# Performance work log

Hardware: AMD Instinct MI355X
Metric: run time of the kernel (lower is better)

The kernel has to match this reference:

```python
import jax, jax.numpy as jnp
import numpy as np

N_CAM = 6
N_HEADS = 8
N_POINTS = 4
D = 256  # internal d_model of the deformable attention


def _sine_pos(h, w, d=D):
    # DETR PositionEmbeddingSine, normalize=True, channels-last (h, w, d)
    npf = d // 2
    two_pi = 2.0 * np.pi
    y = jnp.arange(1, h + 1, dtype=jnp.float32) / (h + 1e-6) * two_pi
    x = jnp.arange(1, w + 1, dtype=jnp.float32) / (w + 1e-6) * two_pi
    dim_t = (10000.0 ** (2.0 * (jnp.arange(npf) // 2) / npf)).astype(jnp.float32)
    def enc(v):
        p = v[:, None] / dim_t
        return jnp.stack([jnp.sin(p[:, 0::2]), jnp.cos(p[:, 1::2])], axis=-1).reshape(v.shape[0], -1)
    py, px = enc(y), enc(x)
    return jnp.concatenate([
        jnp.broadcast_to(py[:, None, :], (h, w, npf)),
        jnp.broadcast_to(px[None, :, :], (h, w, npf))], axis=-1)


def _layernorm(x, g, b, eps=1e-5):
    mu = jnp.mean(x, -1, keepdims=True)
    var = jnp.mean((x - mu) ** 2, -1, keepdims=True)
    return (x - mu) * jax.lax.rsqrt(var + eps) * g + b


def _bilinear_gather(kv, loc_x, loc_y, H, W):
    # kv: (b, L, heads, H*W, c); loc_*: (b, Lq, heads, L, P) normalized to [0,1]
    # emulates F.grid_sample(mode='bilinear', padding_mode='zeros', align_corners=False)
    b, L, heads, HW, c = kv.shape
    _, Lq, _, _, P = loc_x.shape
    x = loc_x * W - 0.5
    y = loc_y * H - 0.5
    x0 = jnp.floor(x)
    y0 = jnp.floor(y)
    fx = x - x0
    fy = y - y0
    out = jnp.zeros((b, Lq, heads, L, P, c), kv.dtype)
    for dx in (0, 1):
        for dy in (0, 1):
            xi = x0 + dx
            yi = y0 + dy
            valid = (xi >= 0) & (xi < W) & (yi >= 0) & (yi < H)
            wgt = (fx if dx else 1.0 - fx) * (fy if dy else 1.0 - fy) * valid
            idx = (jnp.clip(yi, 0, H - 1) * W + jnp.clip(xi, 0, W - 1)).astype(jnp.int32)
            idx_t = idx.transpose(0, 3, 2, 1, 4).reshape(b, L, heads, Lq * P, 1)
            g = jnp.take_along_axis(kv, idx_t, axis=3)
            g = g.reshape(b, L, heads, Lq, P, c).transpose(0, 3, 2, 1, 4, 5)
            out = out + wgt[..., None] * g
    return out  # (b, Lq, heads, L, P, c)


def reference(x, conv0_w, conv0_b, conv2_w, conv2_b, cam_emb,
              off_w, off_b, val_w, val_b, key_w, key_b, out_w, out_b,
              conv1_w, conv1_b, norm0_g, norm0_b,
              lin1_w, lin1_b, lin2_w, lin2_b, norm2_g, norm2_b):
    bn, dim, H, W = x.shape
    b = bn // N_CAM
    hd = D // N_HEADS
    HW = H * W
    Lq = N_CAM * HW

    x_nhwc = x.transpose(0, 2, 3, 1)                  # (bn, H, W, dim)
    residual = x_nhwc.reshape(b, Lq, dim)             # b (n h w) d

    src = (x_nhwc @ conv0_w.T + conv0_b).reshape(b, N_CAM, H, W, D)  # conv0 1x1

    pos = _sine_pos(H, W)                              # (H, W, 256)
    spc = src + pos[None, None] + cam_emb[None, :, None, None, :]
    # per-level global descriptor: mean over pixels of conv2(src+pos+cam)
    g = jnp.mean((spc @ conv2_w.T + conv2_b).reshape(b, N_CAM, HW, D), axis=2)  # (b, n, 256)

    src_flat = src.reshape(b, Lq, D)
    query = spc.reshape(b, Lq, D)                      # src + cam + pos (flattened)

    value = src_flat @ val_w.T + val_b
    keys = src_flat @ key_w.T + key_b

    # sampling locations: per-query reference point + learned offsets (normalized)
    offsets = (query @ off_w.T + off_b).reshape(b, Lq, N_HEADS, N_CAM, N_POINTS, 2)
    ry, rx = jnp.meshgrid(
        (jnp.arange(H, dtype=jnp.float32) + 0.5) / H,
        (jnp.arange(W, dtype=jnp.float32) + 0.5) / W, indexing='ij')
    ref = jnp.tile(jnp.stack([rx.ravel(), ry.ravel()], -1), (N_CAM, 1))  # (Lq, 2) as (x, y)
    loc = ref[None, :, None, None, None, :] + offsets / jnp.array([W, H], jnp.float32)

    # gather keys and values in a single bilinear pass (concat on channel)
    kv = jnp.concatenate([
        keys.reshape(b, N_CAM, HW, N_HEADS, hd),
        value.reshape(b, N_CAM, HW, N_HEADS, hd)], axis=-1).transpose(0, 1, 3, 2, 4)
    sampled = _bilinear_gather(kv, loc[..., 0], loc[..., 1], H, W)  # (b,Lq,heads,L,P,2hd)
    k_s, v_s = sampled[..., :hd], sampled[..., hd:]

    # append per-level global token as an extra key/value point per level
    g_h = g.reshape(b, 1, N_CAM, N_HEADS, hd).transpose(0, 1, 3, 2, 4)[:, :, :, :, None, :]
    g_h = jnp.broadcast_to(g_h, (b, Lq, N_HEADS, N_CAM, 1, hd))
    k_all = jnp.concatenate([k_s, g_h], axis=4)        # (b,Lq,heads,L,P+1,hd)
    v_all = jnp.concatenate([v_s, g_h], axis=4)

    # key-aware attention: softmax over all (level, point) sampled keys
    q_h = query.reshape(b, Lq, N_HEADS, hd)
    logits = jnp.einsum('bqhd,bqhlpd->bqhlp', q_h, k_all) / jnp.sqrt(jnp.float32(hd))
    attn = jax.nn.softmax(logits.reshape(b, Lq, N_HEADS, -1), axis=-1).reshape(logits.shape)
    attn_out = jnp.einsum('bqhlp,bqhlpd->bqhd', attn, v_all).reshape(b, Lq, D)
    attn_out = attn_out @ out_w.T + out_b

    out = attn_out @ conv1_w.T + conv1_b               # conv1 1x1 back to dim
    out = _layernorm(residual + out, norm0_g, norm0_b)
    ffn = jax.nn.relu(out @ lin1_w.T + lin1_b) @ lin2_w.T + lin2_b
    out = _layernorm(out + ffn, norm2_g, norm2_b)

    return out.reshape(b, N_CAM, H, W, dim).transpose(0, 1, 4, 2, 3).reshape(bn, dim, H, W)


def setup_inputs() -> dict:
    key = jax.random.key(0)
    ks = jax.random.split(key, 16)
    B, DIM, H, W = 1, 256, 20, 40

    def w(k, shape, s=0.02):
        return jax.random.normal(k, shape, jnp.float32) * s

    n_off = N_HEADS * N_CAM * N_POINTS * 2
    return {
        "x": jax.random.normal(ks[0], (B * N_CAM, DIM, H, W), jnp.float32),
        "conv0_w": w(ks[1], (D, DIM)), "conv0_b": jnp.zeros((D,), jnp.float32),
        "conv2_w": w(ks[2], (D, D)), "conv2_b": jnp.zeros((D,), jnp.float32),
        "cam_emb": jax.random.uniform(ks[3], (N_CAM, D), jnp.float32),
        "off_w": w(ks[4], (n_off, D)),
        "off_b": jax.random.normal(ks[5], (n_off,), jnp.float32) * 0.5,
        "val_w": w(ks[6], (D, D)), "val_b": jnp.zeros((D,), jnp.float32),
        "key_w": w(ks[7], (D, D)), "key_b": jnp.zeros((D,), jnp.float32),
        "out_w": w(ks[8], (D, D)), "out_b": jnp.zeros((D,), jnp.float32),
        "conv1_w": w(ks[9], (DIM, D)), "conv1_b": jnp.zeros((DIM,), jnp.float32),
        "norm0_g": jnp.ones((DIM,), jnp.float32), "norm0_b": jnp.zeros((DIM,), jnp.float32),
        "lin1_w": w(ks[10], (DIM, DIM)), "lin1_b": jnp.zeros((DIM,), jnp.float32),
        "lin2_w": w(ks[11], (DIM, DIM)), "lin2_b": jnp.zeros((DIM,), jnp.float32),
        "norm2_g": jnp.ones((DIM,), jnp.float32), "norm2_b": jnp.zeros((DIM,), jnp.float32),
    }
```

## Files before the change

### kernel.cpp

```cpp
#include <hip/hip_runtime.h>
#include <math.h>

typedef unsigned short u16;
typedef unsigned int u32;

#define NCAM 6
#define NHEADS 8
#define NPOINTS 4
#define DD 256
#define HH 20
#define WW 40
#define HWSZ 800
#define LQ 4800
#define HDIM 32

typedef __attribute__((ext_vector_type(8))) short bf16x8;
typedef __attribute__((ext_vector_type(4))) float f32x4;

__device__ __forceinline__ u16 f2b(float x) {
    union { float f; u32 u; } v;
    v.f = x;
    u32 r = (v.u + 0x7FFFu + ((v.u >> 16) & 1u)) >> 16;
    return (u16)r;
}
__device__ __forceinline__ float lo2f(u32 u) {
    union { u32 u; float f; } v; v.u = u << 16; return v.f;
}
__device__ __forceinline__ float hi2f(u32 u) {
    union { u32 u; float f; } v; v.u = u & 0xFFFF0000u; return v.f;
}

#define P1_BLOCKS 4022
__global__ __launch_bounds__(256) void prep1(
    const float* __restrict__ x, const float* __restrict__ conv0_w,
    const float* __restrict__ conv0_b, const float* __restrict__ key_w,
    const float* __restrict__ key_b, const float* __restrict__ val_w,
    const float* __restrict__ val_b, const float* __restrict__ off_w,
    const float* __restrict__ off_b, const float* __restrict__ lin1_w,
    const float* __restrict__ lin2_w, const float* __restrict__ conv1_w,
    const float* __restrict__ conv1_b, const float* __restrict__ out_w,
    const float* __restrict__ out_b, const float* __restrict__ cam_emb,
    float* __restrict__ pos, u16* __restrict__ posb, u16* __restrict__ xtb,
    float* __restrict__ mu_x, u16* __restrict__ Wcat, float* __restrict__ bias_cat,
    u16* __restrict__ offwb, u16* __restrict__ lin1b, u16* __restrict__ lin2b,
    u16* __restrict__ wcombb, float* __restrict__ bcomb, float* __restrict__ camoff) {
    int b = blockIdx.x, t = threadIdx.x;
    if (b < 800) {
        int hw = b, d = t;
        int h = hw / WW, w = hw % WW;
        int j = (d & 127) >> 1;
        float dim = powf(10000.0f, (float)j * (1.0f / 64.0f));
        float v;
        if (d < 128) v = (float)(h + 1) / (20.0f + 1e-6f) * (2.0f * (float)M_PI);
        else         v = (float)(w + 1) / (40.0f + 1e-6f) * (2.0f * (float)M_PI);
        float p = v / dim;
        float r = (d & 1) ? cosf(p) : sinf(p);
        pos[hw * DD + d] = r;
        posb[hw * DD + d] = f2b(r);
    } else if (b < 1184) {
        int row = (b - 800) * 4 + (t >> 6);
        int lane = t & 63;
        const float* base = x + (size_t)row * HWSZ;
        float s = 0.f;
        for (int i = lane; i < HWSZ; i += 64) s += base[i];
#pragma unroll
        for (int m = 1; m <= 32; m <<= 1) s += __shfl_xor(s, m);
        if (lane == 0) mu_x[row] = s * (1.0f / (float)HWSZ);
    } else if (b < 2336) {
        int i = (b - 1184) * 256 + t;
        if (i < 65536) {
            Wcat[i] = f2b(conv0_w[i]);
            if (i < 256) bias_cat[i] = conv0_b[i];
        } else if (i < 163840) {
            offwb[i - 65536] = f2b(off_w[i - 65536]);
        } else if (i < 229376) {
            lin1b[i - 163840] = f2b(lin1_w[i - 163840]);
        } else {
            lin2b[i - 229376] = f2b(lin2_w[i - 229376]);
        }
    } else if (b < 2560) {
        int rbase = 256 + (b - 2336) * 4;
        __shared__ float rowv[4][DD];
        __shared__ float cb[DD];
        cb[t] = conv0_b[t];
#pragma unroll
        for (int j = 0; j < 4; ++j) {
            int row = rbase + j;
            const float* srcp;
            if (row < 768) {
                int rj = row - 256;
                int head = rj >> 6, cpair = (rj >> 1) & 31, kv = rj & 1;
                srcp = (kv ? val_w : key_w) + (size_t)(head * 32 + cpair) * DD;
            } else {
                srcp = off_w + (size_t)(row - 768) * DD;
            }
            rowv[j][t] = srcp[t];
        }
        __syncthreads();
        float acc[4] = {0.f, 0.f, 0.f, 0.f};
        for (int c = 0; c < DD; ++c) {
            float w0 = conv0_w[(size_t)c * DD + t];
#pragma unroll
            for (int j = 0; j < 4; ++j) acc[j] += rowv[j][c] * w0;
        }
#pragma unroll
        for (int j = 0; j < 4; ++j) Wcat[(size_t)(rbase + j) * DD + t] = f2b(acc[j]);
        if (t < 4) {
            int row = rbase + t;
            float bb;
            if (row < 768) {
                int rj = row - 256;
                int head = rj >> 6, cpair = (rj >> 1) & 31, kv = rj & 1;
                bb = (kv ? val_b : key_b)[head * 32 + cpair];
            } else {
                bb = off_b[row - 768];
            }
            for (int c = 0; c < DD; ++c) bb += rowv[t][c] * cb[c];
            bias_cat[row] = bb;
        }
    } else if (b < 2816) {
        int n = b - 2560;
        __shared__ float rowv[DD];
        rowv[t] = conv1_w[(size_t)n * DD + t];
        __syncthreads();
        float acc = 0.f;
        for (int m = 0; m < DD; ++m) acc += rowv[m] * out_w[(size_t)m * DD + t];
        wcombb[(size_t)n * DD + t] = f2b(acc);
        if (t == 0) {
            float bb = conv1_b[n];
            for (int m = 0; m < DD; ++m) bb += rowv[m] * out_b[m];
            bcomb[n] = bb;
        }
    } else if (b < 2822) {
        int cam = b - 2816;
        __shared__ float ce[DD];
        ce[t] = cam_emb[cam * DD + t];
        __syncthreads();
        for (int i = t; i < 384; i += 256) {
            float a = 0.f;
            const float* wr = off_w + (size_t)i * DD;
            for (int c = 0; c < DD; ++c) a += ce[c] * wr[c];
            camoff[cam * 384 + i] = a;
        }
    } else {
        int idx = b - 2822;
        int cam = idx / 200, rem = idx % 200;
        int hw0 = (rem % 25) * 32, c0 = (rem / 25) * 32;
        __shared__ float tile[32][33];
        int lhw = t & 31, lc4 = t >> 5;
#pragma unroll
        for (int i = 0; i < 4; ++i) {
            int lc = lc4 * 4 + i;
            tile[lc][lhw] = x[((size_t)(cam * DD + c0 + lc)) * HWSZ + hw0 + lhw];
        }
        __syncthreads();
        int lc2 = t & 31, lhw4 = t >> 5;
#pragma unroll
        for (int i = 0; i < 4; ++i) {
            int lhw2 = lhw4 * 4 + i;
            xtb[((size_t)(cam * HWSZ + hw0 + lhw2)) * DD + c0 + lc2] =
                f2b(tile[lc2][lhw2]);
        }
    }
}

__global__ __launch_bounds__(256) void prep2(
    const u16* __restrict__ posb, const u16* __restrict__ offwb,
    float* __restrict__ posoff, const float* __restrict__ mu_x,
    const float* __restrict__ conv0_w, const float* __restrict__ conv0_b,
    const float* __restrict__ cam_emb, const float* __restrict__ conv2_w,
    const float* __restrict__ conv2_b, float* __restrict__ g) {
    int b = blockIdx.x, t = threadIdx.x;
    if (b < 75) {
        __shared__ __align__(16) u16 As[1056];
        __shared__ __align__(16) u16 Bs[4120];
        int col0 = (b % 3) * 128, row0 = (b / 3) * 32;
        int wv = t >> 6, lane = t & 63;
        int quad = lane >> 4, l = lane & 15;
        f32x4 acc[2][2] = {};
        for (int k0 = 0; k0 < 256; k0 += 32) {
            __syncthreads();
            if (t < 128) {
                int m = t >> 2, j = t & 3;
                *(uint4*)&As[(j * 33 + m) * 8] =
                    *(const uint4*)&posb[(size_t)(row0 + m) * 256 + k0 + j * 8];
            }
            {
                int n = t >> 1, jp = (t & 1) * 2;
                const u16* gsrc = &offwb[(size_t)(col0 + n) * 256 + k0 + jp * 8];
                *(uint4*)&Bs[(jp * 129 + n) * 8]       = *(const uint4*)gsrc;
                *(uint4*)&Bs[((jp + 1) * 129 + n) * 8] = *(const uint4*)(gsrc + 8);
            }
            __syncthreads();
            bf16x8 a0 = *(const bf16x8*)&As[(quad * 33 + l) * 8];
            bf16x8 a1 = *(const bf16x8*)&As[(quad * 33 + 16 + l) * 8];
            bf16x8 b0 = *(const bf16x8*)&Bs[(quad * 129 + wv * 32 + l) * 8];
            bf16x8 b1 = *(const bf16x8*)&Bs[(quad * 129 + wv * 32 + 16 + l) * 8];
            acc[0][0] = __builtin_amdgcn_mfma_f32_16x16x32_bf16(a0, b0, acc[0][0], 0, 0, 0);
            acc[0][1] = __builtin_amdgcn_mfma_f32_16x16x32_bf16(a0, b1, acc[0][1], 0, 0, 0);
            acc[1][0] = __builtin_amdgcn_mfma_f32_16x16x32_bf16(a1, b0, acc[1][0], 0, 0, 0);
            acc[1][1] = __builtin_amdgcn_mfma_f32_16x16x32_bf16(a1, b1, acc[1][1], 0, 0, 0);
        }
#pragma unroll
        for (int mt = 0; mt < 2; ++mt) {
#pragma unroll
            for (int nt = 0; nt < 2; ++nt) {
                int col = col0 + wv * 32 + nt * 16 + l;
#pragma unroll
                for (int r = 0; r < 4; ++r) {
                    int row = row0 + mt * 16 + quad * 4 + r;
                    posoff[(size_t)row * 384 + col] = acc[mt][nt][r];
                }
            }
        }
    } else {
        int cam = b - 75;
        __shared__ float mu[DD];
        __shared__ float smu[DD];
        float pm;
        {
            int d = t;
            int j = (d & 127) >> 1;
            float inv = 1.0f / powf(10000.0f, (float)j * (1.0f / 64.0f));
            float s = 0.f;
            if (d < 128) {
                for (int h = 0; h < HH; ++h) {
                    float p = (float)(h + 1) / (20.0f + 1e-6f) * (2.0f * (float)M_PI) * inv;
                    s += (d & 1) ? cosf(p) : sinf(p);
                }
                pm = s * (1.0f / (float)HH);
            } else {
                for (int w = 0; w < WW; ++w) {
                    float p = (float)(w + 1) / (40.0f + 1e-6f) * (2.0f * (float)M_PI) * inv;
                    s += (d & 1) ? cosf(p) : sinf(p);
                }
                pm = s * (1.0f / (float)WW);
            }
        }
        mu[t] = mu_x[cam * DD + t];
        __syncthreads();
        float a = conv0_b[t] + pm + cam_emb[cam * DD + t];
        const float* wr = conv0_w + (size_t)t * DD;
        for (int k = 0; k < DD; ++k) a += mu[k] * wr[k];
        smu[t] = a;
        __syncthreads();
        float ga = conv2_b[t];
        const float* w2r = conv2_w + (size_t)t * DD;
        for (int d = 0; d < DD; ++d) ga += smu[d] * w2r[d];
        g[cam * DD + t] = ga;
    }
}

__global__ __launch_bounds__(256) void gemm_bf16(
    const u16* __restrict__ Ab, const u16* __restrict__ Wb,
    const float* __restrict__ bias, float* __restrict__ C,
    u16* __restrict__ Cb, int N, int mode) {
    __shared__ __align__(16) u16 As[1056];
    __shared__ __align__(16) u16 Bs[4120];
    int t = threadIdx.x;
    int col0 = blockIdx.x * 128, row0 = blockIdx.y * 32;
    int wv = t >> 6, lane = t & 63;
    int quad = lane >> 4, l = lane & 15;
    f32x4 acc[2][2] = {};
    for (int k0 = 0; k0 < 256; k0 += 32) {
        __syncthreads();
        if (t < 128) {
            int m = t >> 2, j = t & 3;
            *(uint4*)&As[(j * 33 + m) * 8] =
                *(const uint4*)&Ab[(size_t)(row0 + m) * 256 + k0 + j * 8];
        }
        {
            int n = t >> 1, jp = (t & 1) * 2;
            const u16* gsrc = &Wb[(size_t)(col0 + n) * 256 + k0 + jp * 8];
            *(uint4*)&Bs[(jp * 129 + n) * 8]       = *(const uint4*)gsrc;
            *(uint4*)&Bs[((jp + 1) * 129 + n) * 8] = *(const uint4*)(gsrc + 8);
        }
        __syncthreads();
        bf16x8 a0 = *(const bf16x8*)&As[(quad * 33 + l) * 8];
        bf16x8 a1 = *(const bf16x8*)&As[(quad * 33 + 16 + l) * 8];
        bf16x8 b0 = *(const bf16x8*)&Bs[(quad * 129 + wv * 32 + l) * 8];
        bf16x8 b1 = *(const bf16x8*)&Bs[(quad * 129 + wv * 32 + 16 + l) * 8];
        acc[0][0] = __builtin_amdgcn_mfma_f32_16x16x32_bf16(a0, b0, acc[0][0], 0, 0, 0);
        acc[0][1] = __builtin_amdgcn_mfma_f32_16x16x32_bf16(a0, b1, acc[0][1], 0, 0, 0);
        acc[1][0] = __builtin_amdgcn_mfma_f32_16x16x32_bf16(a1, b0, acc[1][0], 0, 0, 0);
        acc[1][1] = __builtin_amdgcn_mfma_f32_16x16x32_bf16(a1, b1, acc[1][1], 0, 0, 0);
    }
#pragma unroll
    for (int mt = 0; mt < 2; ++mt) {
#pragma unroll
        for (int nt = 0; nt < 2; ++nt) {
            int col = col0 + wv * 32 + nt * 16 + l;
            float bb = bias ? bias[col] : 0.f;
#pragma unroll
            for (int r = 0; r < 4; ++r) {
                int row = row0 + mt * 16 + quad * 4 + r;
                float v = acc[mt][nt][r] + bb;
                size_t oi = (size_t)row * N + col;
                if (mode == 0) C[oi] = v;
                else           Cb[oi] = f2b(fmaxf(v, 0.f));
            }
        }
    }
}

__global__ __launch_bounds__(256) void gemm_fused(
    const u16* __restrict__ Ab, const u16* __restrict__ Wcat,
    const float* __restrict__ bias_cat, const float* __restrict__ pos,
    const float* __restrict__ cam_emb, u16* __restrict__ spcb,
    u16* __restrict__ kvcat16, float* __restrict__ offs) {
    __shared__ __align__(16) u16 As[1056];
    __shared__ __align__(16) u16 Bs[4120];
    int t = threadIdx.x;
    int col0 = blockIdx.x * 128, row0 = blockIdx.y * 32;
    int wv = t >> 6, lane = t & 63;
    int quad = lane >> 4, l = lane & 15;
    f32x4 acc[2][2] = {};
    for (int k0 = 0; k0 < 256; k0 += 32) {
        __syncthreads();
        if (t < 128) {
            int m = t >> 2, j = t & 3;
            *(uint4*)&As[(j * 33 + m) * 8] =
                *(const uint4*)&Ab[(size_t)(row0 + m) * 256 + k0 + j * 8];
        }
        {
            int n = t >> 1, jp = (t & 1) * 2;
            const u16* gsrc = &Wcat[(size_t)(col0 + n) * 256 + k0 + jp * 8];
            *(uint4*)&Bs[(jp * 129 + n) * 8]       = *(const uint4*)gsrc;
            *(uint4*)&Bs[((jp + 1) * 129 + n) * 8] = *(const uint4*)(gsrc + 8);
        }
        __syncthreads();
        bf16x8 a0 = *(const bf16x8*)&As[(quad * 33 + l) * 8];
        bf16x8 a1 = *(const bf16x8*)&As[(quad * 33 + 16 + l) * 8];
        bf16x8 b0 = *(const bf16x8*)&Bs[(quad * 129 + wv * 32 + l) * 8];
        bf16x8 b1 = *(const bf16x8*)&Bs[(quad * 129 + wv * 32 + 16 + l) * 8];
        acc[0][0] = __builtin_amdgcn_mfma_f32_16x16x32_bf16(a0, b0, acc[0][0], 0, 0, 0);
        acc[0][1] = __builtin_amdgcn_mfma_f32_16x16x32_bf16(a0, b1, acc[0][1], 0, 0, 0);
        acc[1][0] = __builtin_amdgcn_mfma_f32_16x16x32_bf16(a1, b0, acc[1][0], 0, 0, 0);
        acc[1][1] = __builtin_amdgcn_mfma_f32_16x16x32_bf16(a1, b1, acc[1][1], 0, 0, 0);
    }
#pragma unroll
    for (int mt = 0; mt < 2; ++mt) {
#pragma unroll
        for (int nt = 0; nt < 2; ++nt) {
            int col = col0 + wv * 32 + nt * 16 + l;
            float bb = bias_cat[col];
#pragma unroll
            for (int r = 0; r < 4; ++r) {
                int row = row0 + mt * 16 + quad * 4 + r;
                float v = acc[mt][nt][r] + bb;
                if (col0 < 256) {
                    int cam = row / HWSZ, hw = row % HWSZ;
                    spcb[(size_t)row * 256 + col] =
                        f2b(v + pos[(size_t)hw * 256 + col] + cam_emb[cam * 256 + col]);
                } else if (col0 < 768) {
                    kvcat16[(size_t)row * 512 + (col - 256)] = f2b(v);
                } else {
                    offs[(size_t)row * 384 + (col - 768)] = v;
                }
            }
        }
    }
}

__global__ __launch_bounds__(256, 6) void attn_kernel(
    const u16* __restrict__ spcb, const u16* __restrict__ kvcat16,
    const float* __restrict__ offs, const float* __restrict__ posoff,
    const float* __restrict__ camoff, const float* __restrict__ g,
    u16* __restrict__ attn_out) {
    int qq = blockIdx.x;
    int q0 = qq * 2;
    int tid = threadIdx.x;
    int cam = q0 / HWSZ;
    int hw0 = q0 % HWSZ;
    __shared__ float soff[2][384];
    __shared__ uint2 widx[2][192][4];
    for (int i = tid; i < 768; i += 256) {
        int qi = i / 384, n = i - qi * 384;
        soff[qi][n] = offs[(size_t)(q0 + qi) * 384 + n] +
                      posoff[(size_t)(hw0 + qi) * 384 + n] + camoff[cam * 384 + n];
    }
    __syncthreads();
    for (int e2 = tid; e2 < 384; e2 += 256) {
        int qi = e2 / 192, e = e2 - qi * 192;
        int head = e / 24, r = e - head * 24;
        int scam = r >> 2;
        int hw = hw0 + qi;
        int h = hw / WW, w = hw - h * WW;
        float X = (float)w + soff[qi][e * 2];
        float Y = (float)h + soff[qi][e * 2 + 1];
        float x0f = floorf(X), y0f = floorf(Y);
        float fx = X - x0f, fy = Y - y0f;
        int x0 = (int)x0f, y0 = (int)y0f, x1 = x0 + 1, y1 = y0 + 1;
        float vx0 = (x0 >= 0 && x0 < WW) ? 1.f : 0.f;
        float vx1 = (x1 >= 0 && x1 < WW) ? 1.f : 0.f;
        float vy0 = (y0 >= 0 && y0 < HH) ? 1.f : 0.f;
        float vy1 = (y1 >= 0 && y1 < HH) ? 1.f : 0.f;
        int cx0 = min(max(x0, 0), WW - 1), cx1 = min(max(x1, 0), WW - 1);
        int cy0 = min(max(y0, 0), HH - 1), cy1 = min(max(y1, 0), HH - 1);
        int pb = scam * HWSZ, hb = head * 64;
        widx[qi][e][0] = make_uint2(__float_as_uint((1.f - fx) * (1.f - fy) * vx0 * vy0),
                                    (u32)(((pb + cy0 * WW + cx0) << 9) + hb));
        widx[qi][e][1] = make_uint2(__float_as_uint(fx * (1.f - fy) * vx1 * vy0),
                                    (u32)(((pb + cy0 * WW + cx1) << 9) + hb));
        widx[qi][e][2] = make_uint2(__float_as_uint((1.f - fx) * fy * vx0 * vy1),
                                    (u32)(((pb + cy1 * WW + cx0) << 9) + hb));
        widx[qi][e][3] = make_uint2(__float_as_uint(fx * fy * vx1 * vy1),
                                    (u32)(((pb + cy1 * WW + cx1) << 9) + hb));
    }
    __syncthreads();
    int qi = tid >> 7, head = (tid >> 4) & 7, l = tid & 15;
    int q = q0 + qi;
    int c0 = l * 2;
    u32 qu = *(const u32*)&spcb[(size_t)q * 256 + head * 32 + c0];
    const float scale = 0.17677669529663687f;
    float q0s = lo2f(qu) * scale, q1s = hi2f(qu) * scale;
    float m = -1e30f, den = 0.f, o0 = 0.f, o1 = 0.f;
    for (int sc = 0; sc < NCAM; ++sc) {
        float av0[4], av1[4], lg[4];
#pragma unroll
        for (int p = 0; p < 4; ++p) {
            int e = head * 24 + sc * 4 + p;
            float ak0 = 0.f, ak1 = 0.f, a0 = 0.f, a1 = 0.f;
#pragma unroll
            for (int j = 0; j < 4; ++j) {
                uint2 wi = widx[qi][e][j];
                float wj = __uint_as_float(wi.x);
                int idx = (int)wi.y + 4 * l;
                uint2 d = *(const uint2*)&kvcat16[idx];
                ak0 += wj * lo2f(d.x);
                a0  += wj * hi2f(d.x);
                ak1 += wj * lo2f(d.y);
                a1  += wj * hi2f(d.y);
            }
            av0[p] = a0; av1[p] = a1;
            float pl = q0s * ak0 + q1s * ak1;
            pl += __shfl_xor(pl, 1);
            pl += __shfl_xor(pl, 2);
            pl += __shfl_xor(pl, 4);
            pl += __shfl_xor(pl, 8);
            lg[p] = pl;
        }
        float2 gv = *(const float2*)&g[sc * 256 + head * 32 + c0];
        float pg = q0s * gv.x + q1s * gv.y;
        pg += __shfl_xor(pg, 1);
        pg += __shfl_xor(pg, 2);
        pg += __shfl_xor(pg, 4);
        pg += __shfl_xor(pg, 8);
        float mc = fmaxf(fmaxf(fmaxf(lg[0], lg[1]), fmaxf(lg[2], lg[3])), pg);
        float mn = fmaxf(m, mc);
        float aa = __expf(m - mn);
        float e0p = __expf(lg[0] - mn), e1p = __expf(lg[1] - mn);
        float e2p = __expf(lg[2] - mn), e3p = __expf(lg[3] - mn);
        float e4p = __expf(pg - mn);
        den = den * aa + (e0p + e1p + e2p + e3p + e4p);
        o0 = o0 * aa + e0p * av0[0] + e1p * av0[1] + e2p * av0[2] + e3p * av0[3] + e4p * gv.x;
        o1 = o1 * aa + e0p * av1[0] + e1p * av1[1] + e2p * av1[2] + e3p * av1[3] + e4p * gv.y;
        m = mn;
    }
    float inv = 1.f / den;
    u32 pack = (u32)f2b(o0 * inv) | ((u32)f2b(o1 * inv) << 16);
    *(u32*)&attn_out[(size_t)q * 256 + head * 32 + c0] = pack;
}

__global__ __launch_bounds__(256) void gemm_ln(
    const u16* __restrict__ Ab, const u16* __restrict__ Wb,
    const float* __restrict__ bias, const float* __restrict__ e0_rm,
    const float* __restrict__ x_nchw, const float* __restrict__ gamma,
    const float* __restrict__ beta, float* __restrict__ C_rm,
    u16* __restrict__ Cb, float* __restrict__ C_nchw) {
    __shared__ __align__(16) u16 As[552];
    __shared__ __align__(16) u16 Bs[8232];
    __shared__ float red[4][4][4][2];
    int t = threadIdx.x;
    int row0 = blockIdx.x * 16;
    int wv = t >> 6, lane = t & 63, quad = lane >> 4, l = lane & 15;
    f32x4 acc[4] = {};
    for (int k0 = 0; k0 < 256; k0 += 32) {
        __syncthreads();
        if (t < 64) {
            int mm = t >> 2, j = t & 3;
            *(uint4*)&As[(j * 17 + mm) * 8] =
                *(const uint4*)&Ab[(size_t)(row0 + mm) * 256 + k0 + j * 8];
        }
#pragma unroll
        for (int j = 0; j < 4; ++j)
            *(uint4*)&Bs[(j * 257 + t) * 8] =
                *(const uint4*)&Wb[(size_t)t * 256 + k0 + j * 8];
        __syncthreads();
        bf16x8 a = *(const bf16x8*)&As[(quad * 17 + l) * 8];
#pragma unroll
        for (int nt = 0; nt < 4; ++nt) {
            bf16x8 b = *(const bf16x8*)&Bs[(quad * 257 + wv * 64 + nt * 16 + l) * 8];
            acc[nt] = __builtin_amdgcn_mfma_f32_16x16x32_bf16(a, b, acc[nt], 0, 0, 0);
        }
    }
    int cam = row0 / HWSZ;
    int hw0q = row0 % HWSZ + quad * 4;
    float v[4][4];
    float g4[4], b4[4];
#pragma unroll
    for (int nt = 0; nt < 4; ++nt) {
        int col = wv * 64 + nt * 16 + l;
        float bb = bias[col];
        g4[nt] = gamma[col];
        b4[nt] = beta[col];
        if (x_nchw) {
            float4 rx = *(const float4*)&x_nchw[((size_t)(cam * 256 + col)) * HWSZ + hw0q];
            v[nt][0] = acc[nt][0] + bb + rx.x;
            v[nt][1] = acc[nt][1] + bb + rx.y;
            v[nt][2] = acc[nt][2] + bb + rx.z;
            v[nt][3] = acc[nt][3] + bb + rx.w;
        } else {
#pragma unroll
            for (int r = 0; r < 4; ++r) {
                int row = row0 + quad * 4 + r;
                v[nt][r] = acc[nt][r] + bb + e0_rm[(size_t)row * 256 + col];
            }
        }
    }
#pragma unroll
    for (int r = 0; r < 4; ++r) {
        float s = v[0][r] + v[1][r] + v[2][r] + v[3][r];
        float sq = v[0][r] * v[0][r] + v[1][r] * v[1][r] +
                   v[2][r] * v[2][r] + v[3][r] * v[3][r];
#pragma unroll
        for (int msk = 1; msk <= 8; msk <<= 1) {
            s += __shfl_xor(s, msk);
            sq += __shfl_xor(sq, msk);
        }
        if (l == 0) { red[wv][quad][r][0] = s; red[wv][quad][r][1] = sq; }
    }
    __syncthreads();
    float mean[4], rstd[4];
#pragma unroll
    for (int r = 0; r < 4; ++r) {
        float S = red[0][quad][r][0] + red[1][quad][r][0] +
                  red[2][quad][r][0] + red[3][quad][r][0];
        float Q = red[0][quad][r][1] + red[1][quad][r][1] +
                  red[2][quad][r][1] + red[3][quad][r][1];
        mean[r] = S * (1.0f / 256.0f);
        float var = Q * (1.0f / 256.0f) - mean[r] * mean[r];
        rstd[r] = rsqrtf(var + 1e-5f);
    }
#pragma unroll
    for (int nt = 0; nt < 4; ++nt) {
        int col = wv * 64 + nt * 16 + l;
        if (C_nchw) {
            float4 ov4;
            ov4.x = (v[nt][0] - mean[0]) * rstd[0] * g4[nt] + b4[nt];
            ov4.y = (v[nt][1] - mean[1]) * rstd[1] * g4[nt] + b4[nt];
            ov4.z = (v[nt][2] - mean[2]) * rstd[2] * g4[nt] + b4[nt];
            ov4.w = (v[nt][3] - mean[3]) * rstd[3] * g4[nt] + b4[nt];
            *(float4*)&C_nchw[((size_t)(cam * 256 + col)) * HWSZ + hw0q] = ov4;
        } else {
#pragma unroll
            for (int r = 0; r < 4; ++r) {
                int row = row0 + quad * 4 + r;
                float ov = (v[nt][r] - mean[r]) * rstd[r] * g4[nt] + b4[nt];
                C_rm[(size_t)row * 256 + col] = ov;
                if (Cb) Cb[(size_t)row * 256 + col] = f2b(ov);
            }
        }
    }
}

extern "C" void kernel_launch(void* const* d_in, const int* in_sizes, int n_in,
                              void* d_out, int out_size, void* d_ws, size_t ws_size,
                              hipStream_t stream) {
    const float* x       = (const float*)d_in[0];
    const float* conv0_w = (const float*)d_in[1];
    const float* conv0_b = (const float*)d_in[2];
    const float* conv2_w = (const float*)d_in[3];
    const float* conv2_b = (const float*)d_in[4];
    const float* cam_emb = (const float*)d_in[5];
    const float* off_w   = (const float*)d_in[6];
    const float* off_b   = (const float*)d_in[7];
    const float* val_w   = (const float*)d_in[8];
    const float* val_b   = (const float*)d_in[9];
    const float* key_w   = (const float*)d_in[10];
    const float* key_b   = (const float*)d_in[11];
    const float* out_w   = (const float*)d_in[12];
    const float* out_b   = (const float*)d_in[13];
    const float* conv1_w = (const float*)d_in[14];
    const float* conv1_b = (const float*)d_in[15];
    const float* norm0_g = (const float*)d_in[16];
    const float* norm0_b = (const float*)d_in[17];
    const float* lin1_w  = (const float*)d_in[18];
    const float* lin1_b  = (const float*)d_in[19];
    const float* lin2_w  = (const float*)d_in[20];
    const float* lin2_b  = (const float*)d_in[21];
    const float* norm2_g = (const float*)d_in[22];
    const float* norm2_b = (const float*)d_in[23];

    float* ws = (float*)d_ws;
    const size_t SZ = (size_t)LQ * DD;
    float* pos      = ws;
    float* mu_x     = pos + 204800;
    float* g        = mu_x + 1536;
    float* camoff   = g + 1536;
    float* posoff   = camoff + 2304;
    float* bias_cat = posoff + 307200;
    float* bcomb    = bias_cat + 1152;
    float* offs     = bcomb + 256;
    float* f_posb   = offs + 1843200;
    float* f_xtb    = f_posb + 102400;
    float* f_spcb   = f_xtb + 614400;
    float* f_kvcat  = f_spcb + 614400;
    float* f_Wcat   = f_kvcat + 1228800;
    float* f_offwb  = f_Wcat + 147456;
    float* f_lin1b  = f_offwb + 49152;
    float* f_lin2b  = f_lin1b + 32768;
    float* f_wcombb = f_lin2b + 32768;

    u16* posb    = (u16*)f_posb;
    u16* xtb     = (u16*)f_xtb;
    u16* spcb    = (u16*)f_spcb;
    u16* kvcat16 = (u16*)f_kvcat;
    u16* Wcat    = (u16*)f_Wcat;
    u16* offwb   = (u16*)f_offwb;
    u16* lin1b   = (u16*)f_lin1b;
    u16* lin2b   = (u16*)f_lin2b;
    u16* wcombb  = (u16*)f_wcombb;
    u16*   attn_ob = xtb;
    float* out0    = offs;
    u16*   out0b   = (u16*)(offs + SZ);
    u16*   hidden  = kvcat16;

    prep1<<<P1_BLOCKS, 256, 0, stream>>>(
        x, conv0_w, conv0_b, key_w, key_b, val_w, val_b, off_w, off_b,
        lin1_w, lin2_w, conv1_w, conv1_b, out_w, out_b, cam_emb,
        pos, posb, xtb, mu_x, Wcat, bias_cat, offwb, lin1b, lin2b,
        wcombb, bcomb, camoff);
    prep2<<<81, 256, 0, stream>>>(posb, offwb, posoff, mu_x, conv0_w, conv0_b,
                                  cam_emb, conv2_w, conv2_b, g);
    gemm_fused<<<dim3(9, 150), 256, 0, stream>>>(xtb, Wcat, bias_cat, pos, cam_emb,
                                                 spcb, kvcat16, offs);
    attn_kernel<<<LQ / 2, 256, 0, stream>>>(spcb, kvcat16, offs, posoff, camoff,
                                            g, attn_ob);
    gemm_ln<<<300, 256, 0, stream>>>(attn_ob, wcombb, bcomb, nullptr, x,
                                     norm0_g, norm0_b, out0, out0b, nullptr);
    gemm_bf16<<<dim3(2, 150), 256, 0, stream>>>(out0b, lin1b, lin1_b, nullptr,
                                                hidden, 256, 1);
    gemm_ln<<<300, 256, 0, stream>>>(hidden, lin2b, lin2_b, out0, nullptr,
                                     norm2_g, norm2_b, nullptr, nullptr,
                                     (float*)d_out);
}
```

Before: 243.2 us.

## Fuse FFN stages into single epilogue, separate pos-offset projection, merge prep2 into GEMM

Replaces the full pos@off_w GEMM with separable per-row and per-column projections (posy, posx), using the fact that the sine embedding splits into y and x halves. The g-computation blocks from prep2 are folded into the fused QKV/offset GEMM launch, and the three trailing launches (out projection + LN, lin1, lin2 + LN) are merged into one epilogue kernel that keeps intermediates in shared memory. The attention kernel's packed weight/index shared array is split into two separate arrays. This cuts kernel launches and global round-trips of intermediates, at the cost of a heavier epilogue block with more shared memory and serial GEMMs per block.

```diff
diff --git a/kernel.cpp b/kernel.cpp
--- a/kernel.cpp
+++ b/kernel.cpp
@@ -30,7 +30,7 @@
     union { u32 u; float f; } v; v.u = u & 0xFFFF0000u; return v.f;
 }
 
-#define P1_BLOCKS 4022
+#define P1_BLOCKS 3698
 __global__ __launch_bounds__(256) void prep1(
     const float* __restrict__ x, const float* __restrict__ conv0_w,
     const float* __restrict__ conv0_b, const float* __restrict__ key_w,
@@ -40,10 +40,12 @@
     const float* __restrict__ lin2_w, const float* __restrict__ conv1_w,
     const float* __restrict__ conv1_b, const float* __restrict__ out_w,
     const float* __restrict__ out_b, const float* __restrict__ cam_emb,
-    float* __restrict__ pos, u16* __restrict__ posb, u16* __restrict__ xtb,
-    float* __restrict__ mu_x, u16* __restrict__ Wcat, float* __restrict__ bias_cat,
-    u16* __restrict__ offwb, u16* __restrict__ lin1b, u16* __restrict__ lin2b,
-    u16* __restrict__ wcombb, float* __restrict__ bcomb, float* __restrict__ camoff) {
+    float* __restrict__ pos, u16* __restrict__ xtb, float* __restrict__ mu_x,
+    u16* __restrict__ Wcat, float* __restrict__ bias_cat,
+    u16* __restrict__ lin1b, u16* __restrict__ lin2b,
+    u16* __restrict__ wcombb, float* __restrict__ bcomb,
+    float* __restrict__ camoff, float* __restrict__ posy,
+    float* __restrict__ posx) {
     int b = blockIdx.x, t = threadIdx.x;
     if (b < 800) {
         int hw = b, d = t;
@@ -54,9 +56,7 @@
         if (d < 128) v = (float)(h + 1) / (20.0f + 1e-6f) * (2.0f * (float)M_PI);
         else         v = (float)(w + 1) / (40.0f + 1e-6f) * (2.0f * (float)M_PI);
         float p = v / dim;
-        float r = (d & 1) ? cosf(p) : sinf(p);
-        pos[hw * DD + d] = r;
-        posb[hw * DD + d] = f2b(r);
+        pos[hw * DD + d] = (d & 1) ? cosf(p) : sinf(p);
     } else if (b < 1184) {
         int row = (b - 800) * 4 + (t >> 6);
         int lane = t & 63;
@@ -66,20 +66,18 @@
 #pragma unroll
         for (int m = 1; m <= 32; m <<= 1) s += __shfl_xor(s, m);
         if (lane == 0) mu_x[row] = s * (1.0f / (float)HWSZ);
-    } else if (b < 2336) {
+    } else if (b < 1952) {
         int i = (b - 1184) * 256 + t;
         if (i < 65536) {
             Wcat[i] = f2b(conv0_w[i]);
             if (i < 256) bias_cat[i] = conv0_b[i];
-        } else if (i < 163840) {
-            offwb[i - 65536] = f2b(off_w[i - 65536]);
-        } else if (i < 229376) {
-            lin1b[i - 163840] = f2b(lin1_w[i - 163840]);
+        } else if (i < 131072) {
+            lin1b[i - 65536] = f2b(lin1_w[i - 65536]);
         } else {
-            lin2b[i - 229376] = f2b(lin2_w[i - 229376]);
-        }
-    } else if (b < 2560) {
-        int rbase = 256 + (b - 2336) * 4;
+            lin2b[i - 131072] = f2b(lin2_w[i - 131072]);
+        }
+    } else if (b < 2176) {
+        int rbase = 256 + (b - 1952) * 4;
         __shared__ float rowv[4][DD];
         __shared__ float cb[DD];
         cb[t] = conv0_b[t];
@@ -118,8 +116,8 @@
             for (int c = 0; c < DD; ++c) bb += rowv[t][c] * cb[c];
             bias_cat[row] = bb;
         }
-    } else if (b < 2816) {
-        int n = b - 2560;
+    } else if (b < 2432) {
+        int n = b - 2176;
         __shared__ float rowv[DD];
         rowv[t] = conv1_w[(size_t)n * DD + t];
         __syncthreads();
@@ -131,8 +129,8 @@
             for (int m = 0; m < DD; ++m) bb += rowv[m] * out_b[m];
             bcomb[n] = bb;
         }
-    } else if (b < 2822) {
-        int cam = b - 2816;
+    } else if (b < 2438) {
+        int cam = b - 2432;
         __shared__ float ce[DD];
         ce[t] = cam_emb[cam * DD + t];
         __syncthreads();
@@ -142,8 +140,31 @@
             for (int c = 0; c < DD; ++c) a += ce[c] * wr[c];
             camoff[cam * 384 + i] = a;
         }
+    } else if (b < 2498) {
+        int idx = b - 2438;
+        __shared__ float pv[128];
+        int yside = (idx < 20);
+        int coord = yside ? idx : idx - 20;
+        if (t < 128) {
+            int d = t, j = d >> 1;
+            float dim = powf(10000.0f, (float)j * (1.0f / 64.0f));
+            float v = yside
+                ? (float)(coord + 1) / (20.0f + 1e-6f) * (2.0f * (float)M_PI)
+                : (float)(coord + 1) / (40.0f + 1e-6f) * (2.0f * (float)M_PI);
+            float p = v / dim;
+            pv[d] = (d & 1) ? cosf(p) : sinf(p);
+        }
+        __syncthreads();
+        int koff = yside ? 0 : 128;
+        float* outp = yside ? (posy + coord * 384) : (posx + coord * 384);
+        for (int n = t; n < 384; n += 256) {
+            const float* wr = off_w + (size_t)n * DD + koff;
+            float a = 0.f;
+            for (int d = 0; d < 128; ++d) a += pv[d] * wr[d];
+            outp[n] = a;
+        }
     } else {
-        int idx = b - 2822;
+        int idx = b - 2498;
         int cam = idx / 200, rem = idx % 200;
         int hw0 = (rem % 25) * 32, c0 = (rem / 25) * 32;
         __shared__ float tile[32][33];
@@ -164,17 +185,19 @@
     }
 }
 
-__global__ __launch_bounds__(256) void prep2(
-    const u16* __restrict__ posb, const u16* __restrict__ offwb,
-    float* __restrict__ posoff, const float* __restrict__ mu_x,
-    const float* __restrict__ conv0_w, const float* __restrict__ conv0_b,
-    const float* __restrict__ cam_emb, const float* __restrict__ conv2_w,
+__global__ __launch_bounds__(256) void gemm_fused(
+    const u16* __restrict__ Ab, const u16* __restrict__ Wcat,
+    const float* __restrict__ bias_cat, const float* __restrict__ pos,
+    const float* __restrict__ cam_emb, u16* __restrict__ spcb,
+    u16* __restrict__ kvcat16, float* __restrict__ offs,
+    const float* __restrict__ mu_x, const float* __restrict__ conv0_w,
+    const float* __restrict__ conv0_b, const float* __restrict__ conv2_w,
     const float* __restrict__ conv2_b, float* __restrict__ g) {
     int b = blockIdx.x, t = threadIdx.x;
-    if (b < 75) {
+    if (b < 1350) {
         __shared__ __align__(16) u16 As[1056];
         __shared__ __align__(16) u16 Bs[4120];
-        int col0 = (b % 3) * 128, row0 = (b / 3) * 32;
+        int col0 = (b % 9) * 128, row0 = (b / 9) * 32;
         int wv = t >> 6, lane = t & 63;
         int quad = lane >> 4, l = lane & 15;
         f32x4 acc[2][2] = {};
@@ -183,11 +206,11 @@
             if (t < 128) {
                 int m = t >> 2, j = t & 3;
                 *(uint4*)&As[(j * 33 + m) * 8] =
-                    *(const uint4*)&posb[(size_t)(row0 + m) * 256 + k0 + j * 8];
+                    *(const uint4*)&Ab[(size_t)(row0 + m) * 256 + k0 + j * 8];
             }
             {
                 int n = t >> 1, jp = (t & 1) * 2;
-                const u16* gsrc = &offwb[(size_t)(col0 + n) * 256 + k0 + jp * 8];
+                const u16* gsrc = &Wcat[(size_t)(col0 + n) * 256 + k0 + jp * 8];
                 *(uint4*)&Bs[(jp * 129 + n) * 8]       = *(const uint4*)gsrc;
                 *(uint4*)&Bs[((jp + 1) * 129 + n) * 8] = *(const uint4*)(gsrc + 8);
             }
@@ -206,15 +229,25 @@
 #pragma unroll
             for (int nt = 0; nt < 2; ++nt) {
                 int col = col0 + wv * 32 + nt * 16 + l;
+                float bb = bias_cat[col];
 #pragma unroll
                 for (int r = 0; r < 4; ++r) {
                     int row = row0 + mt * 16 + quad * 4 + r;
-                    posoff[(size_t)row * 384 + col] = acc[mt][nt][r];
+                    float v = acc[mt][nt][r] + bb;
+                    if (col0 < 256) {
+                        int cam = row / HWSZ, hw = row % HWSZ;
+                        spcb[(size_t)row * 256 + col] =
+                            f2b(v + pos[(size_t)hw * 256 + col] + cam_emb[cam * 256 + col]);
+                    } else if (col0 < 768) {
+                        kvcat16[(size_t)row * 512 + (col - 256)] = f2b(v);
+                    } else {
+                        offs[(size_t)row * 384 + (col - 768)] = v;
+                    }
                 }
             }
         }
     } else {
-        int cam = b - 75;
+        int cam = b - 1350;
         __shared__ float mu[DD];
         __shared__ float smu[DD];
         float pm;
@@ -251,133 +284,25 @@
     }
 }
 
-__global__ __launch_bounds__(256) void gemm_bf16(
-    const u16* __restrict__ Ab, const u16* __restrict__ Wb,
-    const float* __restrict__ bias, float* __restrict__ C,
-    u16* __restrict__ Cb, int N, int mode) {
-    __shared__ __align__(16) u16 As[1056];
-    __shared__ __align__(16) u16 Bs[4120];
-    int t = threadIdx.x;
-    int col0 = blockIdx.x * 128, row0 = blockIdx.y * 32;
-    int wv = t >> 6, lane = t & 63;
-    int quad = lane >> 4, l = lane & 15;
-    f32x4 acc[2][2] = {};
-    for (int k0 = 0; k0 < 256; k0 += 32) {
-        __syncthreads();
-        if (t < 128) {
-            int m = t >> 2, j = t & 3;
-            *(uint4*)&As[(j * 33 + m) * 8] =
-                *(const uint4*)&Ab[(size_t)(row0 + m) * 256 + k0 + j * 8];
-        }
-        {
-            int n = t >> 1, jp = (t & 1) * 2;
-            const u16* gsrc = &Wb[(size_t)(col0 + n) * 256 + k0 + jp * 8];
-            *(uint4*)&Bs[(jp * 129 + n) * 8]       = *(const uint4*)gsrc;
-            *(uint4*)&Bs[((jp + 1) * 129 + n) * 8] = *(const uint4*)(gsrc + 8);
-        }
-        __syncthreads();
-        bf16x8 a0 = *(const bf16x8*)&As[(quad * 33 + l) * 8];
-        bf16x8 a1 = *(const bf16x8*)&As[(quad * 33 + 16 + l) * 8];
-        bf16x8 b0 = *(const bf16x8*)&Bs[(quad * 129 + wv * 32 + l) * 8];
-        bf16x8 b1 = *(const bf16x8*)&Bs[(quad * 129 + wv * 32 + 16 + l) * 8];
-        acc[0][0] = __builtin_amdgcn_mfma_f32_16x16x32_bf16(a0, b0, acc[0][0], 0, 0, 0);
-        acc[0][1] = __builtin_amdgcn_mfma_f32_16x16x32_bf16(a0, b1, acc[0][1], 0, 0, 0);
-        acc[1][0] = __builtin_amdgcn_mfma_f32_16x16x32_bf16(a1, b0, acc[1][0], 0, 0, 0);
-        acc[1][1] = __builtin_amdgcn_mfma_f32_16x16x32_bf16(a1, b1, acc[1][1], 0, 0, 0);
-    }
-#pragma unroll
-    for (int mt = 0; mt < 2; ++mt) {
-#pragma unroll
-        for (int nt = 0; nt < 2; ++nt) {
-            int col = col0 + wv * 32 + nt * 16 + l;
-            float bb = bias ? bias[col] : 0.f;
-#pragma unroll
-            for (int r = 0; r < 4; ++r) {
-                int row = row0 + mt * 16 + quad * 4 + r;
-                float v = acc[mt][nt][r] + bb;
-                size_t oi = (size_t)row * N + col;
-                if (mode == 0) C[oi] = v;
-                else           Cb[oi] = f2b(fmaxf(v, 0.f));
-            }
-        }
-    }
-}
-
-__global__ __launch_bounds__(256) void gemm_fused(
-    const u16* __restrict__ Ab, const u16* __restrict__ Wcat,
-    const float* __restrict__ bias_cat, const float* __restrict__ pos,
-    const float* __restrict__ cam_emb, u16* __restrict__ spcb,
-    u16* __restrict__ kvcat16, float* __restrict__ offs) {
-    __shared__ __align__(16) u16 As[1056];
-    __shared__ __align__(16) u16 Bs[4120];
-    int t = threadIdx.x;
-    int col0 = blockIdx.x * 128, row0 = blockIdx.y * 32;
-    int wv = t >> 6, lane = t & 63;
-    int quad = lane >> 4, l = lane & 15;
-    f32x4 acc[2][2] = {};
-    for (int k0 = 0; k0 < 256; k0 += 32) {
-        __syncthreads();
-        if (t < 128) {
-            int m = t >> 2, j = t & 3;
-            *(uint4*)&As[(j * 33 + m) * 8] =
-                *(const uint4*)&Ab[(size_t)(row0 + m) * 256 + k0 + j * 8];
-        }
-        {
-            int n = t >> 1, jp = (t & 1) * 2;
-            const u16* gsrc = &Wcat[(size_t)(col0 + n) * 256 + k0 + jp * 8];
-            *(uint4*)&Bs[(jp * 129 + n) * 8]       = *(const uint4*)gsrc;
-            *(uint4*)&Bs[((jp + 1) * 129 + n) * 8] = *(const uint4*)(gsrc + 8);
-        }
-        __syncthreads();
-        bf16x8 a0 = *(const bf16x8*)&As[(quad * 33 + l) * 8];
-        bf16x8 a1 = *(const bf16x8*)&As[(quad * 33 + 16 + l) * 8];
-        bf16x8 b0 = *(const bf16x8*)&Bs[(quad * 129 + wv * 32 + l) * 8];
-        bf16x8 b1 = *(const bf16x8*)&Bs[(quad * 129 + wv * 32 + 16 + l) * 8];
-        acc[0][0] = __builtin_amdgcn_mfma_f32_16x16x32_bf16(a0, b0, acc[0][0], 0, 0, 0);
-        acc[0][1] = __builtin_amdgcn_mfma_f32_16x16x32_bf16(a0, b1, acc[0][1], 0, 0, 0);
-        acc[1][0] = __builtin_amdgcn_mfma_f32_16x16x32_bf16(a1, b0, acc[1][0], 0, 0, 0);
-        acc[1][1] = __builtin_amdgcn_mfma_f32_16x16x32_bf16(a1, b1, acc[1][1], 0, 0, 0);
-    }
-#pragma unroll
-    for (int mt = 0; mt < 2; ++mt) {
-#pragma unroll
-        for (int nt = 0; nt < 2; ++nt) {
-            int col = col0 + wv * 32 + nt * 16 + l;
-            float bb = bias_cat[col];
-#pragma unroll
-            for (int r = 0; r < 4; ++r) {
-                int row = row0 + mt * 16 + quad * 4 + r;
-                float v = acc[mt][nt][r] + bb;
-                if (col0 < 256) {
-                    int cam = row / HWSZ, hw = row % HWSZ;
-                    spcb[(size_t)row * 256 + col] =
-                        f2b(v + pos[(size_t)hw * 256 + col] + cam_emb[cam * 256 + col]);
-                } else if (col0 < 768) {
-                    kvcat16[(size_t)row * 512 + (col - 256)] = f2b(v);
-                } else {
-                    offs[(size_t)row * 384 + (col - 768)] = v;
-                }
-            }
-        }
-    }
-}
-
 __global__ __launch_bounds__(256, 6) void attn_kernel(
     const u16* __restrict__ spcb, const u16* __restrict__ kvcat16,
-    const float* __restrict__ offs, const float* __restrict__ posoff,
-    const float* __restrict__ camoff, const float* __restrict__ g,
-    u16* __restrict__ attn_out) {
+    const float* __restrict__ offs, const float* __restrict__ posy,
+    const float* __restrict__ posx, const float* __restrict__ camoff,
+    const float* __restrict__ g, u16* __restrict__ attn_out) {
     int qq = blockIdx.x;
     int q0 = qq * 2;
     int tid = threadIdx.x;
     int cam = q0 / HWSZ;
     int hw0 = q0 % HWSZ;
     __shared__ float soff[2][384];
-    __shared__ uint2 widx[2][192][4];
+    __shared__ float wgt[2][192][4];
+    __shared__ int   idxp[2][192][4];
     for (int i = tid; i < 768; i += 256) {
         int qi = i / 384, n = i - qi * 384;
-        soff[qi][n] = offs[(size_t)(q0 + qi) * 384 + n] +
-                      posoff[(size_t)(hw0 + qi) * 384 + n] + camoff[cam * 384 + n];
+        int hw = hw0 + qi;
+        int h = hw / WW, w = hw - h * WW;
+        soff[qi][n] = offs[(size_t)(q0 + qi) * 384 + n] + posy[h * 384 + n] +
+                      posx[w * 384 + n] + camoff[cam * 384 + n];
     }
     __syncthreads();
     for (int e2 = tid; e2 < 384; e2 += 256) {
@@ -397,15 +322,15 @@
         float vy1 = (y1 >= 0 && y1 < HH) ? 1.f : 0.f;
         int cx0 = min(max(x0, 0), WW - 1), cx1 = min(max(x1, 0), WW - 1);
         int cy0 = min(max(y0, 0), HH - 1), cy1 = min(max(y1, 0), HH - 1);
+        wgt[qi][e][0] = (1.f - fx) * (1.f - fy) * vx0 * vy0;
+        wgt[qi][e][1] = fx * (1.f - fy) * vx1 * vy0;
+        wgt[qi][e][2] = (1.f - fx) * fy * vx0 * vy1;
+        wgt[qi][e][3] = fx * fy * vx1 * vy1;
         int pb = scam * HWSZ, hb = head * 64;
-        widx[qi][e][0] = make_uint2(__float_as_uint((1.f - fx) * (1.f - fy) * vx0 * vy0),
-                                    (u32)(((pb + cy0 * WW + cx0) << 9) + hb));
-        widx[qi][e][1] = make_uint2(__float_as_uint(fx * (1.f - fy) * vx1 * vy0),
-                                    (u32)(((pb + cy0 * WW + cx1) << 9) + hb));
-        widx[qi][e][2] = make_uint2(__float_as_uint((1.f - fx) * fy * vx0 * vy1),
-                                    (u32)(((pb + cy1 * WW + cx0) << 9) + hb));
-        widx[qi][e][3] = make_uint2(__float_as_uint(fx * fy * vx1 * vy1),
-                                    (u32)(((pb + cy1 * WW + cx1) << 9) + hb));
+        idxp[qi][e][0] = ((pb + cy0 * WW + cx0) << 9) + hb;
+        idxp[qi][e][1] = ((pb + cy0 * WW + cx1) << 9) + hb;
+        idxp[qi][e][2] = ((pb + cy1 * WW + cx0) << 9) + hb;
+        idxp[qi][e][3] = ((pb + cy1 * WW + cx1) << 9) + hb;
     }
     __syncthreads();
     int qi = tid >> 7, head = (tid >> 4) & 7, l = tid & 15;
@@ -423,9 +348,8 @@
             float ak0 = 0.f, ak1 = 0.f, a0 = 0.f, a1 = 0.f;
 #pragma unroll
             for (int j = 0; j < 4; ++j) {
-                uint2 wi = widx[qi][e][j];
-                float wj = __uint_as_float(wi.x);
-                int idx = (int)wi.y + 4 * l;
+                float wj = wgt[qi][e][j];
+                int idx = idxp[qi][e][j] + 4 * l;
                 uint2 d = *(const uint2*)&kvcat16[idx];
                 ak0 += wj * lo2f(d.x);
                 a0  += wj * hi2f(d.x);
@@ -462,18 +386,24 @@
     *(u32*)&attn_out[(size_t)q * 256 + head * 32 + c0] = pack;
 }
 
-__global__ __launch_bounds__(256) void gemm_ln(
-    const u16* __restrict__ Ab, const u16* __restrict__ Wb,
-    const float* __restrict__ bias, const float* __restrict__ e0_rm,
-    const float* __restrict__ x_nchw, const float* __restrict__ gamma,
-    const float* __restrict__ beta, float* __restrict__ C_rm,
-    u16* __restrict__ Cb, float* __restrict__ C_nchw) {
+__global__ __launch_bounds__(256) void epilogue(
+    const u16* __restrict__ Ab, const u16* __restrict__ Wc,
+    const float* __restrict__ bcomb, const float* __restrict__ x_nchw,
+    const float* __restrict__ n0g, const float* __restrict__ n0b,
+    const u16* __restrict__ W1, const float* __restrict__ b1v,
+    const u16* __restrict__ W2, const float* __restrict__ b2v,
+    const float* __restrict__ n2g, const float* __restrict__ n2b,
+    float* __restrict__ out_nchw) {
     __shared__ __align__(16) u16 As[552];
     __shared__ __align__(16) u16 Bs[8232];
+    __shared__ __align__(16) u16 A2[4360];
     __shared__ float red[4][4][4][2];
     int t = threadIdx.x;
     int row0 = blockIdx.x * 16;
     int wv = t >> 6, lane = t & 63, quad = lane >> 4, l = lane & 15;
+    int cam = row0 / HWSZ;
+    int hw0q = row0 % HWSZ + quad * 4;
+
     f32x4 acc[4] = {};
     for (int k0 = 0; k0 < 256; k0 += 32) {
         __syncthreads();
@@ -485,7 +415,7 @@
 #pragma unroll
         for (int j = 0; j < 4; ++j)
             *(uint4*)&Bs[(j * 257 + t) * 8] =
-                *(const uint4*)&Wb[(size_t)t * 256 + k0 + j * 8];
+                *(const uint4*)&Wc[(size_t)t * 256 + k0 + j * 8];
         __syncthreads();
         bf16x8 a = *(const bf16x8*)&As[(quad * 17 + l) * 8];
 #pragma unroll
@@ -494,29 +424,18 @@
             acc[nt] = __builtin_amdgcn_mfma_f32_16x16x32_bf16(a, b, acc[nt], 0, 0, 0);
         }
     }
-    int cam = row0 / HWSZ;
-    int hw0q = row0 % HWSZ + quad * 4;
     float v[4][4];
-    float g4[4], b4[4];
+    int cols[4];
 #pragma unroll
     for (int nt = 0; nt < 4; ++nt) {
         int col = wv * 64 + nt * 16 + l;
-        float bb = bias[col];
-        g4[nt] = gamma[col];
-        b4[nt] = beta[col];
-        if (x_nchw) {
-            float4 rx = *(const float4*)&x_nchw[((size_t)(cam * 256 + col)) * HWSZ + hw0q];
-            v[nt][0] = acc[nt][0] + bb + rx.x;
-            v[nt][1] = acc[nt][1] + bb + rx.y;
-            v[nt][2] = acc[nt][2] + bb + rx.z;
-            v[nt][3] = acc[nt][3] + bb + rx.w;
-        } else {
-#pragma unroll
-            for (int r = 0; r < 4; ++r) {
-                int row = row0 + quad * 4 + r;
-                v[nt][r] = acc[nt][r] + bb + e0_rm[(size_t)row * 256 + col];
-            }
-        }
+        cols[nt] = col;
+        float bb = bcomb[col];
+        float4 rx = *(const float4*)&x_nchw[((size_t)(cam * 256 + col)) * HWSZ + hw0q];
+        v[nt][0] = acc[nt][0] + bb + rx.x;
+        v[nt][1] = acc[nt][1] + bb + rx.y;
+        v[nt][2] = acc[nt][2] + bb + rx.z;
+        v[nt][3] = acc[nt][3] + bb + rx.w;
     }
 #pragma unroll
     for (int r = 0; r < 4; ++r) {
@@ -531,36 +450,108 @@
         if (l == 0) { red[wv][quad][r][0] = s; red[wv][quad][r][1] = sq; }
     }
     __syncthreads();
-    float mean[4], rstd[4];
+    float o0[4][4];
 #pragma unroll
     for (int r = 0; r < 4; ++r) {
         float S = red[0][quad][r][0] + red[1][quad][r][0] +
                   red[2][quad][r][0] + red[3][quad][r][0];
         float Q = red[0][quad][r][1] + red[1][quad][r][1] +
                   red[2][quad][r][1] + red[3][quad][r][1];
-        mean[r] = S * (1.0f / 256.0f);
-        float var = Q * (1.0f / 256.0f) - mean[r] * mean[r];
-        rstd[r] = rsqrtf(var + 1e-5f);
-    }
+        float mean = S * (1.0f / 256.0f);
+        float var = Q * (1.0f / 256.0f) - mean * mean;
+        float rstd = rsqrtf(var + 1e-5f);
+        int row = quad * 4 + r;
+#pragma unroll
+        for (int nt = 0; nt < 4; ++nt) {
+            int col = cols[nt];
+            float ov = (v[nt][r] - mean) * rstd * n0g[col] + n0b[col];
+            o0[nt][r] = ov;
+            A2[((col >> 3) * 17 + row) * 8 + (col & 7)] = f2b(ov);
+        }
+    }
+    f32x4 acc2[4] = {};
+    for (int k0 = 0; k0 < 256; k0 += 32) {
+        __syncthreads();
+#pragma unroll
+        for (int j = 0; j < 4; ++j)
+            *(uint4*)&Bs[(j * 257 + t) * 8] =
+                *(const uint4*)&W1[(size_t)t * 256 + k0 + j * 8];
+        __syncthreads();
+        bf16x8 a = *(const bf16x8*)&A2[(((k0 >> 3) + quad) * 17 + l) * 8];
+#pragma unroll
+        for (int nt = 0; nt < 4; ++nt) {
+            bf16x8 b = *(const bf16x8*)&Bs[(quad * 257 + wv * 64 + nt * 16 + l) * 8];
+            acc2[nt] = __builtin_amdgcn_mfma_f32_16x16x32_bf16(a, b, acc2[nt], 0, 0, 0);
+        }
+    }
+    __syncthreads();
 #pragma unroll
     for (int nt = 0; nt < 4; ++nt) {
-        int col = wv * 64 + nt * 16 + l;
-        if (C_nchw) {
-            float4 ov4;
-            ov4.x = (v[nt][0] - mean[0]) * rstd[0] * g4[nt] + b4[nt];
-            ov4.y = (v[nt][1] - mean[1]) * rstd[1] * g4[nt] + b4[nt];
-            ov4.z = (v[nt][2] - mean[2]) * rstd[2] * g4[nt] + b4[nt];
-            ov4.w = (v[nt][3] - mean[3]) * rstd[3] * g4[nt] + b4[nt];
-            *(float4*)&C_nchw[((size_t)(cam * 256 + col)) * HWSZ + hw0q] = ov4;
-        } else {
-#pragma unroll
-            for (int r = 0; r < 4; ++r) {
-                int row = row0 + quad * 4 + r;
-                float ov = (v[nt][r] - mean[r]) * rstd[r] * g4[nt] + b4[nt];
-                C_rm[(size_t)row * 256 + col] = ov;
-                if (Cb) Cb[(size_t)row * 256 + col] = f2b(ov);
-            }
-        }
+        int col = cols[nt];
+        float bb = b1v[col];
+#pragma unroll
+        for (int r = 0; r < 4; ++r) {
+            int row = quad * 4 + r;
+            A2[((col >> 3) * 17 + row) * 8 + (col & 7)] = f2b(fmaxf(acc2[nt][r] + bb, 0.f));
+        }
+    }
+    f32x4 acc3[4] = {};
+    for (int k0 = 0; k0 < 256; k0 += 32) {
+        __syncthreads();
+#pragma unroll
+        for (int j = 0; j < 4; ++j)
+            *(uint4*)&Bs[(j * 257 + t) * 8] =
+                *(const uint4*)&W2[(size_t)t * 256 + k0 + j * 8];
+        __syncthreads();
+        bf16x8 a = *(const bf16x8*)&A2[(((k0 >> 3) + quad) * 17 + l) * 8];
+#pragma unroll
+        for (int nt = 0; nt < 4; ++nt) {
+            bf16x8 b = *(const bf16x8*)&Bs[(quad * 257 + wv * 64 + nt * 16 + l) * 8];
+            acc3[nt] = __builtin_amdgcn_mfma_f32_16x16x32_bf16(a, b, acc3[nt], 0, 0, 0);
+        }
+    }
+    float v2[4][4];
+#pragma unroll
+    for (int nt = 0; nt < 4; ++nt) {
+        float bb = b2v[cols[nt]];
+#pragma unroll
+        for (int r = 0; r < 4; ++r) v2[nt][r] = acc3[nt][r] + bb + o0[nt][r];
+    }
+    __syncthreads();
+#pragma unroll
+    for (int r = 0; r < 4; ++r) {
+        float s = v2[0][r] + v2[1][r] + v2[2][r] + v2[3][r];
+        float sq = v2[0][r] * v2[0][r] + v2[1][r] * v2[1][r] +
+                   v2[2][r] * v2[2][r] + v2[3][r] * v2[3][r];
+#pragma unroll
+        for (int msk = 1; msk <= 8; msk <<= 1) {
+            s += __shfl_xor(s, msk);
+            sq += __shfl_xor(sq, msk);
+        }
+        if (l == 0) { red[wv][quad][r][0] = s; red[wv][quad][r][1] = sq; }
+    }
+    __syncthreads();
+    float mean2[4], rstd2[4];
+#pragma unroll
+    for (int r = 0; r < 4; ++r) {
+        float S = red[0][quad][r][0] + red[1][quad][r][0] +
+                  red[2][quad][r][0] + red[3][quad][r][0];
+        float Q = red[0][quad][r][1] + red[1][quad][r][1] +
+                  red[2][quad][r][1] + red[3][quad][r][1];
+        mean2[r] = S * (1.0f / 256.0f);
+        float var = Q * (1.0f / 256.0f) - mean2[r] * mean2[r];
+        rstd2[r] = rsqrtf(var + 1e-5f);
+    }
+#pragma unroll
+    for (int nt = 0; nt < 4; ++nt) {
+        int col = cols[nt];
+        float gg = n2g[col], bb = n2b[col];
+        float4 ov4;
+        ov4.x = (v2[nt][0] - mean2[0]) * rstd2[0] * gg + bb;
+        ov4.y = (v2[nt][1] - mean2[1]) * rstd2[1] * gg + bb;
+        ov4.z = (v2[nt][2] - mean2[2]) * rstd2[2] * gg + bb;
+        ov4.w = (v2[nt][3] - mean2[3]) * rstd2[3] * gg + bb;
+        *(float4*)&out_nchw[((size_t)(cam * 256 + col)) * HWSZ + hw0q] = ov4;
     }
 }
 
@@ -593,55 +584,44 @@
     const float* norm2_b = (const float*)d_in[23];
 
     float* ws = (float*)d_ws;
-    const size_t SZ = (size_t)LQ * DD;
     float* pos      = ws;
     float* mu_x     = pos + 204800;
     float* g        = mu_x + 1536;
     float* camoff   = g + 1536;
-    float* posoff   = camoff + 2304;
-    float* bias_cat = posoff + 307200;
+    float* posy     = camoff + 2304;
+    float* posx     = posy + 7680;
+    float* bias_cat = posx + 15360;
     float* bcomb    = bias_cat + 1152;
     float* offs     = bcomb + 256;
-    float* f_posb   = offs + 1843200;
-    float* f_xtb    = f_posb + 102400;
+    float* f_xtb    = offs + 1843200;
     float* f_spcb   = f_xtb + 614400;
     float* f_kvcat  = f_spcb + 614400;
     float* f_Wcat   = f_kvcat + 1228800;
-    float* f_offwb  = f_Wcat + 147456;
-    float* f_lin1b  = f_offwb + 49152;
+    float* f_lin1b  = f_Wcat + 147456;
     float* f_lin2b  = f_lin1b + 32768;
     float* f_wcombb = f_lin2b + 32768;
 
-    u16* posb    = (u16*)f_posb;
     u16* xtb     = (u16*)f_xtb;
     u16* spcb    = (u16*)f_spcb;
     u16* kvcat16 = (u16*)f_kvcat;
     u16* Wcat    = (u16*)f_Wcat;
-    u16* offwb   = (u16*)f_offwb;
     u16* lin1b   = (u16*)f_lin1b;
     u16* lin2b   = (u16*)f_lin2b;
     u16* wcombb  = (u16*)f_wcombb;
-    u16*   attn_ob = xtb;
-    float* out0    = offs;
-    u16*   out0b   = (u16*)(offs + SZ);
-    u16*   hidden  = kvcat16;
+    u16* attn_ob = xtb;
 
     prep1<<<P1_BLOCKS, 256, 0, stream>>>(
         x, conv0_w, conv0_b, key_w, key_b, val_w, val_b, off_w, off_b,
         lin1_w, lin2_w, conv1_w, conv1_b, out_w, out_b, cam_emb,
-        pos, posb, xtb, mu_x, Wcat, bias_cat, offwb, lin1b, lin2b,
-        wcombb, bcomb, camoff);
-    prep2<<<81, 256, 0, stream>>>(posb, offwb, posoff, mu_x, conv0_w, conv0_b,
-                                  cam_emb, conv2_w, conv2_b, g);
-    gemm_fused<<<dim3(9, 150), 256, 0, stream>>>(xtb, Wcat, bias_cat, pos, cam_emb,
-                                                 spcb, kvcat16, offs);
-    attn_kernel<<<LQ / 2, 256, 0, stream>>>(spcb, kvcat16, offs, posoff, camoff,
-                                            g, attn_ob);
-    gemm_ln<<<300, 256, 0, stream>>>(attn_ob, wcombb, bcomb, nullptr, x,
-                                     norm0_g, norm0_b, out0, out0b, nullptr);
-    gemm_bf16<<<dim3(2, 150), 256, 0, stream>>>(out0b, lin1b, lin1_b, nullptr,
-                                                hidden, 256, 1);
-    gemm_ln<<<300, 256, 0, stream>>>(hidden, lin2b, lin2_b, out0, nullptr,
-                                     norm2_g, norm2_b, nullptr, nullptr,
-                                     (float*)d_out);
-}
+        pos, xtb, mu_x, Wcat, bias_cat, lin1b, lin2b, wcombb, bcomb,
+        camoff, posy, posx);
+    gemm_fused<<<1356, 256, 0, stream>>>(xtb, Wcat, bias_cat, pos, cam_emb,
+                                         spcb, kvcat16, offs, mu_x, conv0_w,
+                                         conv0_b, conv2_w, conv2_b, g);
+    attn_kernel<<<LQ / 2, 256, 0, stream>>>(spcb, kvcat16, offs, posy, posx,
+                                            camoff, g, attn_ob);
+    epilogue<<<300, 256, 0, stream>>>(attn_ob, wcombb, bcomb, x,
+                                      norm0_g, norm0_b, lin1b, lin1_b,
+                                      lin2b, lin2_b, norm2_g, norm2_b,
+                                      (float*)d_out);
+}
```

Measured after the change: 220.3 us. -9.4%, faster.
